# Kernel tuning notes

Measured on AMD Instinct MI355X. Metric: run time of the kernel, lower is better.

The kernel has to match this reference:

```python
import jax, jax.numpy as jnp
import numpy as np

N = 8192
D = 512            # d_model
E = 8              # num_experts
H = 1024           # expert_hidden_dim
RH = 256           # router_hidden_dim
TOPK = 2
IN_DIM = 9 * D + 3
LN_EPS = 1e-5


def layernorm(x, g, b, eps=LN_EPS):
    m = jnp.mean(x, axis=-1, keepdims=True)
    v = jnp.mean((x - m) ** 2, axis=-1, keepdims=True)
    return (x - m) * jax.lax.rsqrt(v + eps) * g + b


def setup_inputs() -> dict:
    key = jax.random.key(0)
    ks = jax.random.split(key, 16)
    s_in = 1.0 / np.sqrt(IN_DIM)
    s_rh = 1.0 / np.sqrt(RH)
    s_h = 1.0 / np.sqrt(H)
    return {
        "z1": jax.random.normal(ks[0], (N, D), jnp.float32),
        "z2": jax.random.normal(ks[1], (N, D), jnp.float32),
        "z3": jax.random.normal(ks[2], (N, D), jnp.float32),
        "mask": jnp.ones((N, 3), jnp.float32),
        # LayerNorms
        "ln_g": jnp.ones((D,), jnp.float32), "ln_b": jnp.zeros((D,), jnp.float32),
        "lnp_g": jnp.ones((D,), jnp.float32), "lnp_b": jnp.zeros((D,), jnp.float32),
        "oln_g": jnp.ones((D,), jnp.float32), "oln_b": jnp.zeros((D,), jnp.float32),
        # Router MLP
        "r_w1": jax.random.normal(ks[3], (IN_DIM, RH), jnp.float32) * s_in,
        "r_b1": jnp.zeros((RH,), jnp.float32),
        "r_w2": jax.random.normal(ks[4], (RH, E), jnp.float32) * s_rh,
        "r_b2": jnp.zeros((E,), jnp.float32),
        "log_temp": jnp.array(np.log(1.0), jnp.float32),
        # Stacked experts: fc1 [E, IN_DIM, H], fc2 [E, H, D]
        "e_w1": jax.random.normal(ks[5], (E, IN_DIM, H), jnp.float32) * s_in,
        "e_b1": jnp.zeros((E, H), jnp.float32),
        "e_w2": jax.random.normal(ks[6], (E, H, D), jnp.float32) * s_h,
        "e_b2": jnp.zeros((E, D), jnp.float32),
    }


def reference(z1, z2, z3, mask, ln_g, ln_b, lnp_g, lnp_b, oln_g, oln_b,
              r_w1, r_b1, r_w2, r_b2, log_temp, e_w1, e_b1, e_w2, e_b2):
    # --- build fusion input ---
    z1n = layernorm(z1, ln_g, ln_b)
    z2n = layernorm(z2, ln_g, ln_b)
    z3n = layernorm(z3, ln_g, ln_b)
    d12 = layernorm(z1n - z2n, lnp_g, lnp_b)
    d13 = layernorm(z1n - z3n, lnp_g, lnp_b)
    d23 = layernorm(z2n - z3n, lnp_g, lnp_b)
    p12 = layernorm(z1n * z2n, lnp_g, lnp_b)
    p13 = layernorm(z1n * z3n, lnp_g, lnp_b)
    p23 = layernorm(z2n * z3n, lnp_g, lnp_b)
    x = jnp.concatenate([z1n, z2n, z3n, d12, d13, d23, p12, p13, p23, mask], axis=-1)  # [N, 9D+3]

    # --- router: MLP + temperature-scaled top-k softmax ---
    temp = jnp.clip(jnp.exp(log_temp), 1e-3, 100.0)
    rh = jax.nn.gelu(x @ r_w1 + r_b1, approximate=False)
    logits = (rh @ r_w2 + r_b2) / temp                      # [N, E]
    topv, topi = jax.lax.top_k(logits, TOPK)
    keep = jnp.zeros_like(logits).at[jnp.arange(logits.shape[0])[:, None], topi].set(1.0)
    masked_logits = jnp.where(keep == 0, -jnp.inf, logits)
    gate = jax.nn.softmax(masked_logits, axis=-1)           # [N, E]

    # --- dense expert compute (matches torch.stack over experts) ---
    eh = jax.nn.gelu(jnp.einsum('ni,eih->neh', x, e_w1) + e_b1, approximate=False)
    outs = jnp.einsum('neh,ehd->ned', eh, e_w2) + e_b2      # [N, E, D]
    z = jnp.einsum('ne,ned->nd', gate, outs)                # combine

    # --- masked residual ---
    denom = jnp.clip(jnp.sum(mask, axis=1, keepdims=True), 1.0, None)
    z_res = (mask[:, 0:1] * z1n + mask[:, 1:2] * z2n + mask[:, 2:3] * z3n) / denom
    z = z + z_res

    return layernorm(z, oln_g, oln_b)
```

## Files before the change

### kernel.cpp

```cpp
#include <hip/hip_runtime.h>
#include <math.h>

#define N_TOK 8192
#define DMODEL 512
#define NEXP 8
#define HEXP 1024
#define RHDIM 256
#define KP 4672
#define IN_REAL 4611
#define BK 64
#define NPAIR (N_TOK * 2)
#define MAXT 136

typedef unsigned short u16;
typedef __bf16 bf16x8 __attribute__((ext_vector_type(8)));
typedef float f32x4 __attribute__((ext_vector_type(4)));

__device__ inline u16 f2bf(float f) {
    union { float f; unsigned u; } x; x.f = f;
    unsigned r = x.u + 0x7FFFu + ((x.u >> 16) & 1u);
    return (u16)(r >> 16);
}
__device__ inline float bf2f(u16 u) {
    union { unsigned u; float f; } x; x.u = ((unsigned)u) << 16;
    return x.f;
}
__device__ inline float gelu_exact(float v) {
    return 0.5f * v * (1.f + erff(v * 0.70710678118654752440f));
}

__device__ inline void async_cp16(const u16* g, u16* l) {
    __builtin_amdgcn_global_load_lds(
        (const __attribute__((address_space(1))) unsigned int*)g,
        (__attribute__((address_space(3))) unsigned int*)l, 16, 0, 0);
}

__device__ inline float2 bstats512(float v, int tid, float* red) {
    float s = v, q = v * v;
    #pragma unroll
    for (int o = 32; o > 0; o >>= 1) {
        s += __shfl_xor(s, o);
        q += __shfl_xor(q, o);
    }
    __syncthreads();
    if ((tid & 63) == 0) { red[(tid >> 6) * 2] = s; red[(tid >> 6) * 2 + 1] = q; }
    __syncthreads();
    if (tid == 0) {
        float S = 0.f, Q = 0.f;
        #pragma unroll
        for (int i = 0; i < 8; i++) { S += red[i * 2]; Q += red[i * 2 + 1]; }
        float m = S * (1.f / 512.f);
        float var = fmaxf(Q * (1.f / 512.f) - m * m, 0.f);
        red[16] = m;
        red[17] = rsqrtf(var + 1e-5f);
    }
    __syncthreads();
    return make_float2(red[16], red[17]);
}

__global__ __launch_bounds__(256)
void transpose_f32_bf16(const float* __restrict__ src, u16* __restrict__ dhi, u16* __restrict__ dlo,
                        int K0, int KPd, int H, size_t sbatch, size_t dbatch) {
    __shared__ float tile[32][33];
    int bz = blockIdx.z;
    src += (size_t)bz * sbatch;
    size_t dob = (size_t)bz * dbatch;
    int k0 = blockIdx.x * 32, h0 = blockIdx.y * 32;
    int tx = threadIdx.x, ty = threadIdx.y;
    for (int i = ty; i < 32; i += 8) {
        int k = k0 + i;
        tile[i][tx] = (k < K0) ? src[(size_t)k * H + (h0 + tx)] : 0.f;
    }
    __syncthreads();
    for (int i = ty; i < 32; i += 8) {
        int h = h0 + i, k = k0 + tx;
        float v = tile[tx][i];
        u16 hv = f2bf(v);
        dhi[dob + (size_t)h * KPd + k] = hv;
        if (dlo) dlo[dob + (size_t)h * KPd + k] = f2bf(v - bf2f(hv));
    }
}

__global__ __launch_bounds__(512)
void build_x(const float* __restrict__ z1, const float* __restrict__ z2, const float* __restrict__ z3,
             const float* __restrict__ mask,
             const float* __restrict__ ln_g, const float* __restrict__ ln_b,
             const float* __restrict__ lnp_g, const float* __restrict__ lnp_b,
             u16* __restrict__ xhi, u16* __restrict__ xlo) {
    __shared__ float red[18];
    int n = blockIdx.x, d = threadIdx.x;
    float a = z1[(size_t)n * DMODEL + d];
    float b = z2[(size_t)n * DMODEL + d];
    float c = z3[(size_t)n * DMODEL + d];
    float gg = ln_g[d], bb = ln_b[d], pg = lnp_g[d], pb = lnp_b[d];
    size_t base = (size_t)n * KP;

    auto emit = [&](int seg, float v) {
        u16 h = f2bf(v);
        xhi[base + seg * DMODEL + d] = h;
        xlo[base + seg * DMODEL + d] = f2bf(v - bf2f(h));
    };
    float2 s;
    s = bstats512(a, d, red); float z1n = (a - s.x) * s.y * gg + bb;
    s = bstats512(b, d, red); float z2n = (b - s.x) * s.y * gg + bb;
    s = bstats512(c, d, red); float z3n = (c - s.x) * s.y * gg + bb;
    emit(0, z1n); emit(1, z2n); emit(2, z3n);
    auto pln = [&](int seg, float v) {
        float2 st = bstats512(v, d, red);
        emit(seg, (v - st.x) * st.y * pg + pb);
    };
    pln(3, z1n - z2n); pln(4, z1n - z3n); pln(5, z2n - z3n);
    pln(6, z1n * z2n); pln(7, z1n * z3n); pln(8, z2n * z3n);
    if (d < 64) {
        int col = 9 * DMODEL + d;
        float v = (d < 3) ? mask[(size_t)n * 3 + d] : 0.f;
        u16 h = f2bf(v);
        xhi[base + col] = h;
        xlo[base + col] = f2bf(v - bf2f(h));
    }
}


#define GEMM_DEFS                                                             \
    int t = threadIdx.x;                                                      \
    int lane = t & 63, w = t >> 6;                                            \
    int r8 = lane >> 3;                                                       \
    int ce = ((lane & 7) ^ r8) * 8;         \
    int fr = lane & 15, q4 = lane >> 4;                                       \
    int wm = (w & 1) * 64, wn = (w >> 1) * 64;                                \
    f32x4 acc[4][4];                                                          \
    { f32x4 z4 = {0.f, 0.f, 0.f, 0.f};                                        \
      _Pragma("unroll") for (int i = 0; i < 4; i++)                           \
      _Pragma("unroll") for (int j = 0; j < 4; j++) acc[i][j] = z4; }         \
    u16* lA0 = lA + (w * 16) * BK;                                            \
    u16* lA1 = lA + (w * 16 + 8) * BK;                                        \
    u16* lB0 = lB + (w * 32) * BK;                                            \
    u16* lB1 = lB + (w * 32 + 8) * BK;                                        \
    u16* lB2 = lB + (w * 32 + 16) * BK;                                       \
    u16* lB3 = lB + (w * 32 + 24) * BK;

#define GEMM_KSTEP                                                            \
        __syncthreads();                                                      \
        async_cp16(gA0, lA0); async_cp16(gA1, lA1);                           \
        async_cp16(gB0, lB0); async_cp16(gB1, lB1);                           \
        async_cp16(gB2, lB2); async_cp16(gB3, lB3);                           \
        gA0 += BK; gA1 += BK; gB0 += BK; gB1 += BK; gB2 += BK; gB3 += BK;     \
        __syncthreads();                                                      \
        _Pragma("unroll") for (int ks = 0; ks < 2; ks++) {                    \
            bf16x8 af[4], bfr[4];                                             \
            int cofs = (((q4 + ks * 4) ^ (fr & 7)) * 8);                      \
            _Pragma("unroll") for (int i = 0; i < 4; i++)                     \
                af[i] = *(const bf16x8*)&lA[(wm + i * 16 + fr) * BK + cofs];  \
            _Pragma("unroll") for (int j = 0; j < 4; j++)                     \
                bfr[j] = *(const bf16x8*)&lB[(wn + j * 16 + fr) * BK + cofs]; \
            _Pragma("unroll") for (int i = 0; i < 4; i++)                     \
            _Pragma("unroll") for (int j = 0; j < 4; j++)                     \
                acc[i][j] = __builtin_amdgcn_mfma_f32_16x16x32_bf16(af[i], bfr[j], acc[i][j], 0, 0, 0); \
        }

__global__ __launch_bounds__(512, 4)
void router_fc1(const u16* __restrict__ xhi, const u16* __restrict__ xlo,
                const u16* __restrict__ rw1hi, const u16* __restrict__ rw1lo,
                float* __restrict__ rpart) {
    int part = blockIdx.x >> 6, mt = blockIdx.x & 63;
    int region = part >> 1, half = part & 1;
    const u16* A = (region == 2) ? xlo : xhi;
    const u16* B = (region == 1) ? rw1lo : rw1hi;
    int kbase = half ? 2304 : 0;
    int klen  = half ? 2368 : 2304;

    __shared__ u16 lA[128 * BK];
    __shared__ u16 lB[256 * BK];
    GEMM_DEFS

    const u16* gA0 = A + (size_t)(mt * 128 + w * 16 + r8) * KP + kbase + ce;
    const u16* gA1 = A + (size_t)(mt * 128 + w * 16 + 8 + r8) * KP + kbase + ce;
    const u16* gB0 = B + (size_t)(w * 32 + r8) * KP + kbase + ce;
    const u16* gB1 = B + (size_t)(w * 32 + 8 + r8) * KP + kbase + ce;
    const u16* gB2 = B + (size_t)(w * 32 + 16 + r8) * KP + kbase + ce;
    const u16* gB3 = B + (size_t)(w * 32 + 24 + r8) * KP + kbase + ce;

    for (int k0 = 0; k0 < klen; k0 += BK) {
        GEMM_KSTEP
    }
    float* outp = rpart + (size_t)part * ((size_t)N_TOK * RHDIM);
    int cn = lane & 15;
    #pragma unroll
    for (int i = 0; i < 4; i++)
        #pragma unroll
        for (int rr = 0; rr < 4; rr++) {
            int mg = mt * 128 + wm + i * 16 + q4 * 4 + rr;
            #pragma unroll
            for (int j = 0; j < 4; j++)
                outp[(size_t)mg * RHDIM + wn + j * 16 + cn] = acc[i][j][rr];
        }
}

__global__ void router_act(const float* __restrict__ rpart, const float* __restrict__ r_b1,
                           float* __restrict__ rh) {
    int idx = blockIdx.x * 256 + threadIdx.x;
    float v = 0.f;
    #pragma unroll
    for (int p = 0; p < 6; p++) v += rpart[(size_t)p * ((size_t)N_TOK * RHDIM) + idx];
    v += r_b1[idx & (RHDIM - 1)];
    rh[idx] = gelu_exact(v);
}

__global__ __launch_bounds__(256)
void logits_topk(const float* __restrict__ rh, const float* __restrict__ r_w2,
                 const float* __restrict__ r_b2, const float* __restrict__ log_temp,
                 float* __restrict__ pgate, int* __restrict__ pexp,
                 int* __restrict__ lists, int* __restrict__ counts) {
    int t = threadIdx.x, wave = t >> 6, lane = t & 63;
    int n = blockIdx.x * 4 + wave;
    int e = lane & 7, ch = lane >> 3;
    const float* r = rh + (size_t)n * RHDIM;
    float s = 0.f;
    #pragma unroll
    for (int k = 0; k < 32; k++) s += r[ch * 32 + k] * r_w2[(ch * 32 + k) * 8 + e];
    s += __shfl_xor(s, 8);
    s += __shfl_xor(s, 16);
    s += __shfl_xor(s, 32);
    float temp = fminf(fmaxf(expf(log_temp[0]), 1e-3f), 100.f);
    float logit = (s + r_b2[e]) / temp;
    float l[8];
    #pragma unroll
    for (int i = 0; i < 8; i++) l[i] = __shfl(logit, i);
    if (lane == 0) {
        int i1 = 0;
        #pragma unroll
        for (int i = 1; i < 8; i++) if (l[i] > l[i1]) i1 = i;
        int i2 = (i1 == 0) ? 1 : 0;
        #pragma unroll
        for (int i = 0; i < 8; i++) if (i != i1 && l[i] > l[i2]) i2 = i;
        float p = expf(l[i2] - l[i1]);
        float g1 = 1.f / (1.f + p);
        float g2 = p / (1.f + p);
        pgate[n * 2] = g1;     pexp[n * 2] = i1;
        pgate[n * 2 + 1] = g2; pexp[n * 2 + 1] = i2;
        int pos1 = atomicAdd(&counts[i1], 1);
        lists[(size_t)i1 * N_TOK + pos1] = n * 2;
        int pos2 = atomicAdd(&counts[i2], 1);
        lists[(size_t)i2 * N_TOK + pos2] = n * 2 + 1;
    }
}

__global__ void sched_tiles(const int* __restrict__ counts, int* __restrict__ tiles) {
    if (threadIdx.x == 0) {
        int rem[NEXP], t = 0;
        for (int e = 0; e < NEXP; e++) rem[e] = (counts[e] + 127) >> 7;
        for (int mt = 0; mt < MAXT; mt++)
            for (int e = 0; e < NEXP; e++)
                if (mt < rem[e]) tiles[t++] = (e << 16) | mt;
        for (; t < MAXT; t++) tiles[t] = -1;
    }
}

__global__ __launch_bounds__(512, 4)
void expert_fc1(const u16* __restrict__ xhi, const u16* __restrict__ w1t,
                const float* __restrict__ e_b1, const int* __restrict__ lists,
                const int* __restrict__ counts, const int* __restrict__ tiles,
                u16* __restrict__ eh) {
    int ti = blockIdx.x % MAXT, nt = blockIdx.x / MAXT;
    int info = tiles[ti];
    if (info < 0) return;
    int e = info >> 16, mt = info & 0xFFFF;
    int cnt = counts[e];

    __shared__ u16 lA[128 * BK];
    __shared__ u16 lB[256 * BK];
    __shared__ int rows[128];
    int tt = threadIdx.x;
    if (tt < 128) {
        int m = mt * 128 + tt;
        rows[tt] = lists[(size_t)e * N_TOK + (m < cnt ? m : 0)];
    }
    __syncthreads();

    GEMM_DEFS

    const u16* gA0 = xhi + (size_t)(rows[w * 16 + r8] >> 1) * KP + ce;
    const u16* gA1 = xhi + (size_t)(rows[w * 16 + 8 + r8] >> 1) * KP + ce;
    const u16* wb = w1t + (size_t)e * HEXP * KP + (size_t)(nt * 256) * KP;
    const u16* gB0 = wb + (size_t)(w * 32 + r8) * KP + ce;
    const u16* gB1 = wb + (size_t)(w * 32 + 8 + r8) * KP + ce;
    const u16* gB2 = wb + (size_t)(w * 32 + 16 + r8) * KP + ce;
    const u16* gB3 = wb + (size_t)(w * 32 + 24 + r8) * KP + ce;

    for (int k0 = 0; k0 < KP; k0 += BK) {
        GEMM_KSTEP
    }
    int cn = lane & 15;
    #pragma unroll
    for (int i = 0; i < 4; i++)
        #pragma unroll
        for (int rr = 0; rr < 4; rr++) {
            int ml = wm + i * 16 + q4 * 4 + rr;
            int mg = mt * 128 + ml;
            if (mg < cnt) {
                int entry = rows[ml];
                #pragma unroll
                for (int j = 0; j < 4; j++) {
                    int col = nt * 256 + wn + j * 16 + cn;
                    float v = acc[i][j][rr] + e_b1[(size_t)e * HEXP + col];
                    eh[(size_t)entry * HEXP + col] = f2bf(gelu_exact(v));
                }
            }
        }
}

__global__ __launch_bounds__(512, 4)
void expert_fc2(const u16* __restrict__ eh, const u16* __restrict__ w2t,
                const int* __restrict__ lists, const int* __restrict__ counts,
                const int* __restrict__ tiles, float* __restrict__ outs) {
    int ti = blockIdx.x % MAXT, nt = blockIdx.x / MAXT;
    int info = tiles[ti];
    if (info < 0) return;
    int e = info >> 16, mt = info & 0xFFFF;
    int cnt = counts[e];

    __shared__ u16 lA[128 * BK];
    __shared__ u16 lB[256 * BK];
    __shared__ int rows[128];
    int tt = threadIdx.x;
    if (tt < 128) {
        int m = mt * 128 + tt;
        rows[tt] = lists[(size_t)e * N_TOK + (m < cnt ? m : 0)];
    }
    __syncthreads();

    GEMM_DEFS

    const u16* gA0 = eh + (size_t)rows[w * 16 + r8] * HEXP + ce;
    const u16* gA1 = eh + (size_t)rows[w * 16 + 8 + r8] * HEXP + ce;
    const u16* wb = w2t + (size_t)e * DMODEL * HEXP + (size_t)(nt * 256) * HEXP;
    const u16* gB0 = wb + (size_t)(w * 32 + r8) * HEXP + ce;
    const u16* gB1 = wb + (size_t)(w * 32 + 8 + r8) * HEXP + ce;
    const u16* gB2 = wb + (size_t)(w * 32 + 16 + r8) * HEXP + ce;
    const u16* gB3 = wb + (size_t)(w * 32 + 24 + r8) * HEXP + ce;

    for (int k0 = 0; k0 < HEXP; k0 += BK) {
        GEMM_KSTEP
    }
    int cn = lane & 15;
    #pragma unroll
    for (int i = 0; i < 4; i++)
        #pragma unroll
        for (int rr = 0; rr < 4; rr++) {
            int ml = wm + i * 16 + q4 * 4 + rr;
            int mg = mt * 128 + ml;
            if (mg < cnt) {
                int entry = rows[ml];
                #pragma unroll
                for (int j = 0; j < 4; j++) {
                    int col = nt * 256 + wn + j * 16 + cn;
                    outs[(size_t)entry * DMODEL + col] = acc[i][j][rr];
                }
            }
        }
}

__global__ __launch_bounds__(512)
void combine_ln(const float* __restrict__ outs, const float* __restrict__ pgate,
                const int* __restrict__ pexp, const float* __restrict__ e_b2,
                const float* __restrict__ mask, const u16* __restrict__ xhi,
                const u16* __restrict__ xlo, const float* __restrict__ oln_g,
                const float* __restrict__ oln_b, float* __restrict__ out) {
    __shared__ float red[18];
    int n = blockIdx.x, d = threadIdx.x;
    float g0 = pgate[n * 2], g1 = pgate[n * 2 + 1];
    int e0 = pexp[n * 2], e1 = pexp[n * 2 + 1];
    float o = g0 * (outs[(size_t)(n * 2) * DMODEL + d] + e_b2[(size_t)e0 * DMODEL + d])
            + g1 * (outs[(size_t)(n * 2 + 1) * DMODEL + d] + e_b2[(size_t)e1 * DMODEL + d]);
    float m0 = mask[n * 3 + 0], m1 = mask[n * 3 + 1], m2 = mask[n * 3 + 2];
    float denom = fmaxf(m0 + m1 + m2, 1.f);
    size_t xb = (size_t)n * KP;
    float z1n = bf2f(xhi[xb + d]) + bf2f(xlo[xb + d]);
    float z2n = bf2f(xhi[xb + DMODEL + d]) + bf2f(xlo[xb + DMODEL + d]);
    float z3n = bf2f(xhi[xb + 2 * DMODEL + d]) + bf2f(xlo[xb + 2 * DMODEL + d]);
    float z = o + (m0 * z1n + m1 * z2n + m2 * z3n) / denom;
    float2 st = bstats512(z, d, red);
    out[(size_t)n * DMODEL + d] = (z - st.x) * st.y * oln_g[d] + oln_b[d];
}

extern "C" void kernel_launch(void* const* d_in, const int* in_sizes, int n_in,
                              void* d_out, int out_size, void* d_ws, size_t ws_size,
                              hipStream_t stream) {
    (void)in_sizes; (void)n_in; (void)out_size; (void)ws_size;
    const float* z1       = (const float*)d_in[0];
    const float* z2       = (const float*)d_in[1];
    const float* z3       = (const float*)d_in[2];
    const float* mask     = (const float*)d_in[3];
    const float* ln_g     = (const float*)d_in[4];
    const float* ln_b     = (const float*)d_in[5];
    const float* lnp_g    = (const float*)d_in[6];
    const float* lnp_b    = (const float*)d_in[7];
    const float* oln_g    = (const float*)d_in[8];
    const float* oln_b    = (const float*)d_in[9];
    const float* r_w1     = (const float*)d_in[10];
    const float* r_b1     = (const float*)d_in[11];
    const float* r_w2     = (const float*)d_in[12];
    const float* r_b2     = (const float*)d_in[13];
    const float* log_temp = (const float*)d_in[14];
    const float* e_w1     = (const float*)d_in[15];
    const float* e_b1     = (const float*)d_in[16];
    const float* e_w2     = (const float*)d_in[17];
    const float* e_b2     = (const float*)d_in[18];
    float* out = (float*)d_out;

    char* p = (char*)d_ws;
    auto carve = [&](size_t bytes) { char* r = p; p += (bytes + 255) & ~(size_t)255; return r; };
    u16*   xhi    = (u16*)carve((size_t)N_TOK * KP * 2);
    u16*   xlo    = (u16*)carve((size_t)N_TOK * KP * 2);
    u16*   w1t    = (u16*)carve((size_t)NEXP * HEXP * KP * 2);
    u16*   w2t    = (u16*)carve((size_t)NEXP * DMODEL * HEXP * 2);
    u16*   rw1hi  = (u16*)carve((size_t)RHDIM * KP * 2);
    u16*   rw1lo  = (u16*)carve((size_t)RHDIM * KP * 2);
    float* rpart  = (float*)carve((size_t)6 * N_TOK * RHDIM * 4);
    float* rh     = (float*)carve((size_t)N_TOK * RHDIM * 4);
    u16*   eh     = (u16*)carve((size_t)NPAIR * HEXP * 2);
    float* outsb  = (float*)carve((size_t)NPAIR * DMODEL * 4);
    float* pgate  = (float*)carve((size_t)NPAIR * 4);
    int*   pexp   = (int*)carve((size_t)NPAIR * 4);
    int*   lists  = (int*)carve((size_t)NEXP * N_TOK * 4);
    int*   counts = (int*)carve(256);
    int*   tiles  = (int*)carve(MAXT * 4);

    dim3 tb(32, 8);
    transpose_f32_bf16<<<dim3(KP / 32, HEXP / 32, NEXP), tb, 0, stream>>>(
        e_w1, w1t, (u16*)nullptr, IN_REAL, KP, HEXP, (size_t)IN_REAL * HEXP, (size_t)HEXP * KP);
    transpose_f32_bf16<<<dim3(HEXP / 32, DMODEL / 32, NEXP), tb, 0, stream>>>(
        e_w2, w2t, (u16*)nullptr, HEXP, HEXP, DMODEL, (size_t)HEXP * DMODEL, (size_t)DMODEL * HEXP);
    transpose_f32_bf16<<<dim3(KP / 32, RHDIM / 32, 1), tb, 0, stream>>>(
        r_w1, rw1hi, rw1lo, IN_REAL, KP, RHDIM, (size_t)0, (size_t)0);

    build_x<<<N_TOK, 512, 0, stream>>>(z1, z2, z3, mask, ln_g, ln_b, lnp_g, lnp_b, xhi, xlo);

    router_fc1<<<384, 512, 0, stream>>>(xhi, xlo, rw1hi, rw1lo, rpart);
    router_act<<<(N_TOK * RHDIM) / 256, 256, 0, stream>>>(rpart, r_b1, rh);

    hipMemsetAsync(counts, 0, 256, stream);
    logits_topk<<<N_TOK / 4, 256, 0, stream>>>(rh, r_w2, r_b2, log_temp, pgate, pexp, lists, counts);
    sched_tiles<<<1, 64, 0, stream>>>(counts, tiles);

    expert_fc1<<<MAXT * 4, 512, 0, stream>>>(xhi, w1t, e_b1, lists, counts, tiles, eh);
    expert_fc2<<<MAXT * 2, 512, 0, stream>>>(eh, w2t, lists, counts, tiles, outsb);

    combine_ln<<<N_TOK, 512, 0, stream>>>(outsb, pgate, pexp, e_b2, mask, xhi, xlo, oln_g, oln_b, out);
}
```

Baseline: 1.043 ms.

## Shrink GEMM tiles to 128x128, fuse router activation, batch LN reductions

The GEMM kernels (router fc1, expert fc1/fc2) move from 512-thread 128x256 tiles to 256-thread 128x128 tiles, doubling the block count, and the block index ordering is changed so that neighbouring blocks share the same row tile. The router_act kernel is removed: logits_topk now sums the partial results, adds the bias and applies GELU itself, which drops one launch and one round trip of the rh buffer. build_x batches its nine LayerNorm statistic reductions into two multi-value block reductions instead of nine serial ones, and sched_tiles now orders tiles expert-major instead of interleaving experts. The smaller tiles give more parallelism and finer load balance, but each loaded A element is reused across fewer output columns, so operand traffic per FLOP goes up.

```diff
diff --git a/kernel.cpp b/kernel.cpp
--- a/kernel.cpp
+++ b/kernel.cpp
@@ -33,6 +33,29 @@
     __builtin_amdgcn_global_load_lds(
         (const __attribute__((address_space(1))) unsigned int*)g,
         (__attribute__((address_space(3))) unsigned int*)l, 16, 0, 0);
+}
+
+template<int M>
+__device__ inline void breduce(float (&v)[M], int tid, float* red) {
+    #pragma unroll
+    for (int o = 32; o > 0; o >>= 1)
+        #pragma unroll
+        for (int i = 0; i < M; i++) v[i] += __shfl_xor(v[i], o);
+    __syncthreads();
+    if ((tid & 63) == 0) {
+        #pragma unroll
+        for (int i = 0; i < M; i++) red[(tid >> 6) * M + i] = v[i];
+    }
+    __syncthreads();
+    if (tid < M) {
+        float S = 0.f;
+        #pragma unroll
+        for (int w8 = 0; w8 < 8; w8++) S += red[w8 * M + tid];
+        red[96 + tid] = S;
+    }
+    __syncthreads();
+    #pragma unroll
+    for (int i = 0; i < M; i++) v[i] = red[96 + i];
 }
 
 __device__ inline float2 bstats512(float v, int tid, float* red) {
@@ -87,7 +110,7 @@
              const float* __restrict__ ln_g, const float* __restrict__ ln_b,
              const float* __restrict__ lnp_g, const float* __restrict__ lnp_b,
              u16* __restrict__ xhi, u16* __restrict__ xlo) {
-    __shared__ float red[18];
+    __shared__ float red[108];
     int n = blockIdx.x, d = threadIdx.x;
     float a = z1[(size_t)n * DMODEL + d];
     float b = z2[(size_t)n * DMODEL + d];
@@ -100,17 +123,28 @@
         xhi[base + seg * DMODEL + d] = h;
         xlo[base + seg * DMODEL + d] = f2bf(v - bf2f(h));
     };
-    float2 s;
-    s = bstats512(a, d, red); float z1n = (a - s.x) * s.y * gg + bb;
-    s = bstats512(b, d, red); float z2n = (b - s.x) * s.y * gg + bb;
-    s = bstats512(c, d, red); float z3n = (c - s.x) * s.y * gg + bb;
+    auto lnv = [](float v, float s, float q, float g, float bo) {
+        float m = s * (1.f / 512.f);
+        float var = fmaxf(q * (1.f / 512.f) - m * m, 0.f);
+        return (v - m) * rsqrtf(var + 1e-5f) * g + bo;
+    };
+    float v6[6] = {a, a * a, b, b * b, c, c * c};
+    breduce<6>(v6, d, red);
+    float z1n = lnv(a, v6[0], v6[1], gg, bb);
+    float z2n = lnv(b, v6[2], v6[3], gg, bb);
+    float z3n = lnv(c, v6[4], v6[5], gg, bb);
     emit(0, z1n); emit(1, z2n); emit(2, z3n);
-    auto pln = [&](int seg, float v) {
-        float2 st = bstats512(v, d, red);
-        emit(seg, (v - st.x) * st.y * pg + pb);
-    };
-    pln(3, z1n - z2n); pln(4, z1n - z3n); pln(5, z2n - z3n);
-    pln(6, z1n * z2n); pln(7, z1n * z3n); pln(8, z2n * z3n);
+    float d12 = z1n - z2n, d13 = z1n - z3n, d23 = z2n - z3n;
+    float p12 = z1n * z2n, p13 = z1n * z3n, p23 = z2n * z3n;
+    float v12[12] = {d12, d12 * d12, d13, d13 * d13, d23, d23 * d23,
+                     p12, p12 * p12, p13, p13 * p13, p23, p23 * p23};
+    breduce<12>(v12, d, red);
+    emit(3, lnv(d12, v12[0], v12[1], pg, pb));
+    emit(4, lnv(d13, v12[2], v12[3], pg, pb));
+    emit(5, lnv(d23, v12[4], v12[5], pg, pb));
+    emit(6, lnv(p12, v12[6], v12[7], pg, pb));
+    emit(7, lnv(p13, v12[8], v12[9], pg, pb));
+    emit(8, lnv(p23, v12[10], v12[11], pg, pb));
     if (d < 64) {
         int col = 9 * DMODEL + d;
         float v = (d < 3) ? mask[(size_t)n * 3 + d] : 0.f;
@@ -132,19 +166,18 @@
     { f32x4 z4 = {0.f, 0.f, 0.f, 0.f};                                        \
       _Pragma("unroll") for (int i = 0; i < 4; i++)                           \
       _Pragma("unroll") for (int j = 0; j < 4; j++) acc[i][j] = z4; }         \
-    u16* lA0 = lA + (w * 16) * BK;                                            \
-    u16* lA1 = lA + (w * 16 + 8) * BK;                                        \
-    u16* lB0 = lB + (w * 32) * BK;                                            \
-    u16* lB1 = lB + (w * 32 + 8) * BK;                                        \
-    u16* lB2 = lB + (w * 32 + 16) * BK;                                       \
-    u16* lB3 = lB + (w * 32 + 24) * BK;
+    u16 *lAp[4], *lBp[4];                                                     \
+    _Pragma("unroll") for (int i = 0; i < 4; i++) {                           \
+        lAp[i] = lA + (w * 32 + 8 * i) * BK;                                  \
+        lBp[i] = lB + (w * 32 + 8 * i) * BK;                                  \
+    }
 
 #define GEMM_KSTEP                                                            \
         __syncthreads();                                                      \
-        async_cp16(gA0, lA0); async_cp16(gA1, lA1);                           \
-        async_cp16(gB0, lB0); async_cp16(gB1, lB1);                           \
-        async_cp16(gB2, lB2); async_cp16(gB3, lB3);                           \
-        gA0 += BK; gA1 += BK; gB0 += BK; gB1 += BK; gB2 += BK; gB3 += BK;     \
+        _Pragma("unroll") for (int i = 0; i < 4; i++) {                       \
+            async_cp16(gA[i], lAp[i]); async_cp16(gB[i], lBp[i]);             \
+            gA[i] += BK; gB[i] += BK;                                         \
+        }                                                                     \
         __syncthreads();                                                      \
         _Pragma("unroll") for (int ks = 0; ks < 2; ks++) {                    \
             bf16x8 af[4], bfr[4];                                             \
@@ -158,11 +191,11 @@
                 acc[i][j] = __builtin_amdgcn_mfma_f32_16x16x32_bf16(af[i], bfr[j], acc[i][j], 0, 0, 0); \
         }
 
-__global__ __launch_bounds__(512, 4)
+__global__ __launch_bounds__(256, 4)
 void router_fc1(const u16* __restrict__ xhi, const u16* __restrict__ xlo,
                 const u16* __restrict__ rw1hi, const u16* __restrict__ rw1lo,
                 float* __restrict__ rpart) {
-    int part = blockIdx.x >> 6, mt = blockIdx.x & 63;
+    int nt = blockIdx.x & 1, mt = (blockIdx.x >> 1) & 63, part = blockIdx.x >> 7;
     int region = part >> 1, half = part & 1;
     const u16* A = (region == 2) ? xlo : xhi;
     const u16* B = (region == 1) ? rw1lo : rw1hi;
@@ -170,15 +203,15 @@
     int klen  = half ? 2368 : 2304;
 
     __shared__ u16 lA[128 * BK];
-    __shared__ u16 lB[256 * BK];
+    __shared__ u16 lB[128 * BK];
     GEMM_DEFS
 
-    const u16* gA0 = A + (size_t)(mt * 128 + w * 16 + r8) * KP + kbase + ce;
-    const u16* gA1 = A + (size_t)(mt * 128 + w * 16 + 8 + r8) * KP + kbase + ce;
-    const u16* gB0 = B + (size_t)(w * 32 + r8) * KP + kbase + ce;
-    const u16* gB1 = B + (size_t)(w * 32 + 8 + r8) * KP + kbase + ce;
-    const u16* gB2 = B + (size_t)(w * 32 + 16 + r8) * KP + kbase + ce;
-    const u16* gB3 = B + (size_t)(w * 32 + 24 + r8) * KP + kbase + ce;
+    const u16* gA[4]; const u16* gB[4];
+    #pragma unroll
+    for (int i = 0; i < 4; i++) {
+        gA[i] = A + (size_t)(mt * 128 + w * 32 + 8 * i + r8) * KP + kbase + ce;
+        gB[i] = B + (size_t)(nt * 128 + w * 32 + 8 * i + r8) * KP + kbase + ce;
+    }
 
     for (int k0 = 0; k0 < klen; k0 += BK) {
         GEMM_KSTEP
@@ -192,41 +225,44 @@
             int mg = mt * 128 + wm + i * 16 + q4 * 4 + rr;
             #pragma unroll
             for (int j = 0; j < 4; j++)
-                outp[(size_t)mg * RHDIM + wn + j * 16 + cn] = acc[i][j][rr];
+                outp[(size_t)mg * RHDIM + nt * 128 + wn + j * 16 + cn] = acc[i][j][rr];
         }
 }
 
-__global__ void router_act(const float* __restrict__ rpart, const float* __restrict__ r_b1,
-                           float* __restrict__ rh) {
-    int idx = blockIdx.x * 256 + threadIdx.x;
-    float v = 0.f;
-    #pragma unroll
-    for (int p = 0; p < 6; p++) v += rpart[(size_t)p * ((size_t)N_TOK * RHDIM) + idx];
-    v += r_b1[idx & (RHDIM - 1)];
-    rh[idx] = gelu_exact(v);
-}
-
 __global__ __launch_bounds__(256)
-void logits_topk(const float* __restrict__ rh, const float* __restrict__ r_w2,
-                 const float* __restrict__ r_b2, const float* __restrict__ log_temp,
+void logits_topk(const float* __restrict__ rpart, const float* __restrict__ r_b1,
+                 const float* __restrict__ r_w2, const float* __restrict__ r_b2,
+                 const float* __restrict__ log_temp,
                  float* __restrict__ pgate, int* __restrict__ pexp,
                  int* __restrict__ lists, int* __restrict__ counts) {
     int t = threadIdx.x, wave = t >> 6, lane = t & 63;
     int n = blockIdx.x * 4 + wave;
-    int e = lane & 7, ch = lane >> 3;
-    const float* r = rh + (size_t)n * RHDIM;
-    float s = 0.f;
-    #pragma unroll
-    for (int k = 0; k < 32; k++) s += r[ch * 32 + k] * r_w2[(ch * 32 + k) * 8 + e];
-    s += __shfl_xor(s, 8);
-    s += __shfl_xor(s, 16);
-    s += __shfl_xor(s, 32);
-    float temp = fminf(fmaxf(expf(log_temp[0]), 1e-3f), 100.f);
-    float logit = (s + r_b2[e]) / temp;
-    float l[8];
-    #pragma unroll
-    for (int i = 0; i < 8; i++) l[i] = __shfl(logit, i);
+    float4 v = {0.f, 0.f, 0.f, 0.f};
+    #pragma unroll
+    for (int p = 0; p < 6; p++) {
+        float4 s = ((const float4*)(rpart + (size_t)p * ((size_t)N_TOK * RHDIM) + (size_t)n * RHDIM))[lane];
+        v.x += s.x; v.y += s.y; v.z += s.z; v.w += s.w;
+    }
+    float4 b1 = ((const float4*)r_b1)[lane];
+    float rh0 = gelu_exact(v.x + b1.x);
+    float rh1 = gelu_exact(v.y + b1.y);
+    float rh2 = gelu_exact(v.z + b1.z);
+    float rh3 = gelu_exact(v.w + b1.w);
+    int k = lane * 4;
+    float p8[8];
+    #pragma unroll
+    for (int e = 0; e < 8; e++)
+        p8[e] = rh0 * r_w2[(k + 0) * 8 + e] + rh1 * r_w2[(k + 1) * 8 + e]
+              + rh2 * r_w2[(k + 2) * 8 + e] + rh3 * r_w2[(k + 3) * 8 + e];
+    #pragma unroll
+    for (int o = 32; o > 0; o >>= 1)
+        #pragma unroll
+        for (int e = 0; e < 8; e++) p8[e] += __shfl_xor(p8[e], o);
     if (lane == 0) {
+        float temp = fminf(fmaxf(expf(log_temp[0]), 1e-3f), 100.f);
+        float l[8];
+        #pragma unroll
+        for (int e = 0; e < 8; e++) l[e] = (p8[e] + r_b2[e]) / temp;
         int i1 = 0;
         #pragma unroll
         for (int i = 1; i < 8; i++) if (l[i] > l[i1]) i1 = i;
@@ -247,28 +283,28 @@
 
 __global__ void sched_tiles(const int* __restrict__ counts, int* __restrict__ tiles) {
     if (threadIdx.x == 0) {
-        int rem[NEXP], t = 0;
-        for (int e = 0; e < NEXP; e++) rem[e] = (counts[e] + 127) >> 7;
-        for (int mt = 0; mt < MAXT; mt++)
-            for (int e = 0; e < NEXP; e++)
-                if (mt < rem[e]) tiles[t++] = (e << 16) | mt;
-        for (; t < MAXT; t++) tiles[t] = -1;
-    }
-}
-
-__global__ __launch_bounds__(512, 4)
+        int tcount = 0;
+        for (int e = 0; e < NEXP; e++) {
+            int nt = (counts[e] + 127) >> 7;
+            for (int mt = 0; mt < nt; mt++) tiles[tcount++] = (e << 16) | mt;
+        }
+        for (; tcount < MAXT; tcount++) tiles[tcount] = -1;
+    }
+}
+
+__global__ __launch_bounds__(256, 4)
 void expert_fc1(const u16* __restrict__ xhi, const u16* __restrict__ w1t,
                 const float* __restrict__ e_b1, const int* __restrict__ lists,
                 const int* __restrict__ counts, const int* __restrict__ tiles,
                 u16* __restrict__ eh) {
-    int ti = blockIdx.x % MAXT, nt = blockIdx.x / MAXT;
+    int nt = blockIdx.x & 7, ti = blockIdx.x >> 3;
     int info = tiles[ti];
     if (info < 0) return;
     int e = info >> 16, mt = info & 0xFFFF;
     int cnt = counts[e];
 
     __shared__ u16 lA[128 * BK];
-    __shared__ u16 lB[256 * BK];
+    __shared__ u16 lB[128 * BK];
     __shared__ int rows[128];
     int tt = threadIdx.x;
     if (tt < 128) {
@@ -279,13 +315,13 @@
 
     GEMM_DEFS
 
-    const u16* gA0 = xhi + (size_t)(rows[w * 16 + r8] >> 1) * KP + ce;
-    const u16* gA1 = xhi + (size_t)(rows[w * 16 + 8 + r8] >> 1) * KP + ce;
-    const u16* wb = w1t + (size_t)e * HEXP * KP + (size_t)(nt * 256) * KP;
-    const u16* gB0 = wb + (size_t)(w * 32 + r8) * KP + ce;
-    const u16* gB1 = wb + (size_t)(w * 32 + 8 + r8) * KP + ce;
-    const u16* gB2 = wb + (size_t)(w * 32 + 16 + r8) * KP + ce;
-    const u16* gB3 = wb + (size_t)(w * 32 + 24 + r8) * KP + ce;
+    const u16* wb = w1t + (size_t)e * HEXP * KP + (size_t)(nt * 128) * KP;
+    const u16* gA[4]; const u16* gB[4];
+    #pragma unroll
+    for (int i = 0; i < 4; i++) {
+        gA[i] = xhi + (size_t)(rows[w * 32 + 8 * i + r8] >> 1) * KP + ce;
+        gB[i] = wb + (size_t)(w * 32 + 8 * i + r8) * KP + ce;
+    }
 
     for (int k0 = 0; k0 < KP; k0 += BK) {
         GEMM_KSTEP
@@ -301,7 +337,7 @@
                 int entry = rows[ml];
                 #pragma unroll
                 for (int j = 0; j < 4; j++) {
-                    int col = nt * 256 + wn + j * 16 + cn;
+                    int col = nt * 128 + wn + j * 16 + cn;
                     float v = acc[i][j][rr] + e_b1[(size_t)e * HEXP + col];
                     eh[(size_t)entry * HEXP + col] = f2bf(gelu_exact(v));
                 }
@@ -309,18 +345,18 @@
         }
 }
 
-__global__ __launch_bounds__(512, 4)
+__global__ __launch_bounds__(256, 4)
 void expert_fc2(const u16* __restrict__ eh, const u16* __restrict__ w2t,
                 const int* __restrict__ lists, const int* __restrict__ counts,
                 const int* __restrict__ tiles, float* __restrict__ outs) {
-    int ti = blockIdx.x % MAXT, nt = blockIdx.x / MAXT;
+    int nt = blockIdx.x & 3, ti = blockIdx.x >> 2;
     int info = tiles[ti];
     if (info < 0) return;
     int e = info >> 16, mt = info & 0xFFFF;
     int cnt = counts[e];
 
     __shared__ u16 lA[128 * BK];
-    __shared__ u16 lB[256 * BK];
+    __shared__ u16 lB[128 * BK];
     __shared__ int rows[128];
     int tt = threadIdx.x;
     if (tt < 128) {
@@ -331,13 +367,13 @@
 
     GEMM_DEFS
 
-    const u16* gA0 = eh + (size_t)rows[w * 16 + r8] * HEXP + ce;
-    const u16* gA1 = eh + (size_t)rows[w * 16 + 8 + r8] * HEXP + ce;
-    const u16* wb = w2t + (size_t)e * DMODEL * HEXP + (size_t)(nt * 256) * HEXP;
-    const u16* gB0 = wb + (size_t)(w * 32 + r8) * HEXP + ce;
-    const u16* gB1 = wb + (size_t)(w * 32 + 8 + r8) * HEXP + ce;
-    const u16* gB2 = wb + (size_t)(w * 32 + 16 + r8) * HEXP + ce;
-    const u16* gB3 = wb + (size_t)(w * 32 + 24 + r8) * HEXP + ce;
+    const u16* wb = w2t + (size_t)e * DMODEL * HEXP + (size_t)(nt * 128) * HEXP;
+    const u16* gA[4]; const u16* gB[4];
+    #pragma unroll
+    for (int i = 0; i < 4; i++) {
+        gA[i] = eh + (size_t)rows[w * 32 + 8 * i + r8] * HEXP + ce;
+        gB[i] = wb + (size_t)(w * 32 + 8 * i + r8) * HEXP + ce;
+    }
 
     for (int k0 = 0; k0 < HEXP; k0 += BK) {
         GEMM_KSTEP
@@ -353,7 +389,7 @@
                 int entry = rows[ml];
                 #pragma unroll
                 for (int j = 0; j < 4; j++) {
-                    int col = nt * 256 + wn + j * 16 + cn;
+                    int col = nt * 128 + wn + j * 16 + cn;
                     outs[(size_t)entry * DMODEL + col] = acc[i][j][rr];
                 }
             }
@@ -417,7 +453,6 @@
     u16*   rw1hi  = (u16*)carve((size_t)RHDIM * KP * 2);
     u16*   rw1lo  = (u16*)carve((size_t)RHDIM * KP * 2);
     float* rpart  = (float*)carve((size_t)6 * N_TOK * RHDIM * 4);
-    float* rh     = (float*)carve((size_t)N_TOK * RHDIM * 4);
     u16*   eh     = (u16*)carve((size_t)NPAIR * HEXP * 2);
     float* outsb  = (float*)carve((size_t)NPAIR * DMODEL * 4);
     float* pgate  = (float*)carve((size_t)NPAIR * 4);
@@ -436,15 +471,15 @@
 
     build_x<<<N_TOK, 512, 0, stream>>>(z1, z2, z3, mask, ln_g, ln_b, lnp_g, lnp_b, xhi, xlo);
 
-    router_fc1<<<384, 512, 0, stream>>>(xhi, xlo, rw1hi, rw1lo, rpart);
-    router_act<<<(N_TOK * RHDIM) / 256, 256, 0, stream>>>(rpart, r_b1, rh);
+    router_fc1<<<768, 256, 0, stream>>>(xhi, xlo, rw1hi, rw1lo, rpart);
 
     hipMemsetAsync(counts, 0, 256, stream);
-    logits_topk<<<N_TOK / 4, 256, 0, stream>>>(rh, r_w2, r_b2, log_temp, pgate, pexp, lists, counts);
+    logits_topk<<<N_TOK / 4, 256, 0, stream>>>(rpart, r_b1, r_w2, r_b2, log_temp,
+                                               pgate, pexp, lists, counts);
     sched_tiles<<<1, 64, 0, stream>>>(counts, tiles);
 
-    expert_fc1<<<MAXT * 4, 512, 0, stream>>>(xhi, w1t, e_b1, lists, counts, tiles, eh);
-    expert_fc2<<<MAXT * 2, 512, 0, stream>>>(eh, w2t, lists, counts, tiles, outsb);
+    expert_fc1<<<MAXT * 8, 256, 0, stream>>>(xhi, w1t, e_b1, lists, counts, tiles, eh);
+    expert_fc2<<<MAXT * 4, 256, 0, stream>>>(eh, w2t, lists, counts, tiles, outsb);
 
     combine_ln<<<N_TOK, 512, 0, stream>>>(outsb, pgate, pexp, e_b2, mask, xhi, xlo, oln_g, oln_b, out);
 }
```

Measured after the change: 1.009 ms. 1.03x faster.
